# Kernel optimization log

Hardware: AMD Instinct MI355X
Metric: run time of the kernel (lower is better)

The kernel has to match this reference:

```python
import jax, jax.numpy as jnp
import numpy as np

B, T, C, H, D = 2, 2048, 1024, 16, 64

def setup_inputs() -> dict:
    key = jax.random.key(0)
    ks = jax.random.split(key, 5)
    s = 1.0 / np.sqrt(C)
    return {
        "hidden_states": jax.random.normal(ks[0], (B, T, C), jnp.float32),
        "Wq": jax.random.normal(ks[1], (H, C, D), jnp.float32) * s,
        "Wk": jax.random.normal(ks[2], (H, C, D), jnp.float32) * s,
        "Wv": jax.random.normal(ks[3], (H, C, D), jnp.float32) * s,
        "Wo": jax.random.normal(ks[4], (C, C), jnp.float32) * s,
    }

def reference(hidden_states, Wq, Wk, Wv, Wo):
    x = hidden_states  # (B, T, C)
    q = jnp.einsum("btc,hcd->bhtd", x, Wq)
    k = jnp.einsum("btc,hcd->bhtd", x, Wk)
    v = jnp.einsum("btc,hcd->bhtd", x, Wv)
    scale = 1.0 / jnp.sqrt(jnp.asarray(D, x.dtype))
    scores = jnp.einsum("bhtd,bhsd->bhts", q, k) * scale  # (B,H,T,T)
    Tlen = x.shape[1]
    causal = jnp.tril(jnp.ones((Tlen, Tlen), bool))
    scores = jnp.where(causal, scores, jnp.asarray(-jnp.inf, x.dtype))
    probs = jax.nn.softmax(scores, axis=-1)
    heads = jnp.einsum("bhts,bhsd->bhtd", probs, v)  # (B,H,T,D)
    concat = heads.transpose(0, 2, 1, 3).reshape(x.shape[0], Tlen, H * D)  # (B,T,C)
    return jnp.einsum("btc,oc->bto", concat, Wo)  # output projection (dropout=0)
```

## Files before the change

### kernel.cpp

```cpp
#include <hip/hip_runtime.h>
#include <math.h>

#define B_ 2
#define T_ 2048
#define C_ 1024
#define H_ 16
#define D_ 64

typedef short short8 __attribute__((ext_vector_type(8)));
typedef float f32x4 __attribute__((ext_vector_type(4)));

#define LOG2E 1.44269504088896f

__device__ __forceinline__ unsigned short f2bf(float f) {
    unsigned int u = __float_as_uint(f);
    u += 0x7FFFu + ((u >> 16) & 1u);
    return (unsigned short)(u >> 16);
}

#define NCAST 2560

__global__ __launch_bounds__(256) void prep_all(
    const float* __restrict__ x,  const float* __restrict__ Wq,
    const float* __restrict__ Wk, const float* __restrict__ Wv,
    const float* __restrict__ Wo,
    unsigned short* __restrict__ xb,   unsigned short* __restrict__ Wall,
    unsigned short* __restrict__ wob,  int nX, int nW)
{
    const int bid = blockIdx.x;
    const int tid = threadIdx.x;
    if (bid < NCAST) {
        int i = (bid * 256 + tid) * 8;
        const float* s;
        unsigned short* d;
        if (i < nX) { s = x + i; d = xb + i; }
        else {
            int j = i - nX;
            if (j >= nW) return;
            s = Wo + j; d = wob + j;
        }
        float4 a = *(const float4*)s;
        float4 b = *(const float4*)(s + 4);
        ushort4 o0, o1;
        o0.x = f2bf(a.x); o0.y = f2bf(a.y); o0.z = f2bf(a.z); o0.w = f2bf(a.w);
        o1.x = f2bf(b.x); o1.y = f2bf(b.y); o1.z = f2bf(b.z); o1.w = f2bf(b.w);
        *(ushort4*)d = o0;
        *(ushort4*)(d + 4) = o1;
        return;
    }
    __shared__ float t[64][65];
    const int tb = bid - NCAST;
    const int c0 = (tb & 15) * 64;
    const int h  = (tb >> 4) & 15;
    const int z  = tb >> 8;
    const float* W = (z == 0) ? Wq : (z == 1) ? Wk : Wv;
    unsigned short* Wt = Wall + (size_t)z * H_ * D_ * C_;
    const int r = tid >> 4, c4 = (tid & 15) * 4;
    #pragma unroll
    for (int p = 0; p < 4; p++) {
        int cl = r + p * 16;
        float4 v = *(const float4*)&W[((size_t)h * C_ + c0 + cl) * D_ + c4];
        t[cl][c4 + 0] = v.x; t[cl][c4 + 1] = v.y;
        t[cl][c4 + 2] = v.z; t[cl][c4 + 3] = v.w;
    }
    __syncthreads();
    #pragma unroll
    for (int p = 0; p < 4; p++) {
        int d = r + p * 16;
        ushort4 o;
        o.x = f2bf(t[c4 + 0][d]); o.y = f2bf(t[c4 + 1][d]);
        o.z = f2bf(t[c4 + 2][d]); o.w = f2bf(t[c4 + 3][d]);
        *(ushort4*)&Wt[((size_t)h * D_ + d) * C_ + c0 + c4] = o;
    }
}

__global__ __launch_bounds__(256) void qkv_big(
    const unsigned short* __restrict__ X,
    const unsigned short* __restrict__ Wall,
    unsigned short* __restrict__ Qo,
    unsigned short* __restrict__ Ko,
    unsigned short* __restrict__ Vt)
{
    __shared__ unsigned short As[128][72];
    __shared__ unsigned short Bs[128][72];

    const int m0 = blockIdx.x * 128;
    const int n0 = blockIdx.y * 128;
    const int z  = n0 >> 10;
    const int tid = threadIdx.x;
    const int w = tid >> 6, lane = tid & 63, quad = lane >> 4, l16 = lane & 15;
    const int wm = w & 1, wn = w >> 1;
    const int lrow = tid >> 3, lcol = (tid & 7) * 8;

    f32x4 acc[4][4] = {};

    short8 ar[4], br[4];
    #pragma unroll
    for (int p = 0; p < 4; p++) {
        int r = lrow + p * 32;
        ar[p] = *(const short8*)&X[(size_t)(m0 + r) * C_ + lcol];
        br[p] = *(const short8*)&Wall[(size_t)(n0 + r) * C_ + lcol];
    }

    for (int k0 = 0; k0 < C_; k0 += 64) {
        __syncthreads();
        #pragma unroll
        for (int p = 0; p < 4; p++) {
            int r = lrow + p * 32;
            *(short8*)&As[r][lcol] = ar[p];
            *(short8*)&Bs[r][lcol] = br[p];
        }
        __syncthreads();
        if (k0 + 64 < C_) {
            #pragma unroll
            for (int p = 0; p < 4; p++) {
                int r = lrow + p * 32;
                ar[p] = *(const short8*)&X[(size_t)(m0 + r) * C_ + k0 + 64 + lcol];
                br[p] = *(const short8*)&Wall[(size_t)(n0 + r) * C_ + k0 + 64 + lcol];
            }
        }
        #pragma unroll
        for (int ks = 0; ks < 2; ks++) {
            short8 af[4], bf[4];
            #pragma unroll
            for (int i = 0; i < 4; i++)
                af[i] = *(const short8*)&As[wm * 64 + i * 16 + l16][ks * 32 + quad * 8];
            #pragma unroll
            for (int j = 0; j < 4; j++)
                bf[j] = *(const short8*)&Bs[wn * 64 + j * 16 + l16][ks * 32 + quad * 8];
            #pragma unroll
            for (int i = 0; i < 4; i++)
                #pragma unroll
                for (int j = 0; j < 4; j++)
                    acc[i][j] = __builtin_amdgcn_mfma_f32_16x16x32_bf16(af[i], bf[j], acc[i][j], 0, 0, 0);
        }
    }

    if (z == 2) {
        #pragma unroll
        for (int j = 0; j < 4; j++) {
            const int n = n0 + wn * 64 + j * 16 + l16;
            const int h = (n >> 6) & 15, d = n & 63;
            #pragma unroll
            for (int i = 0; i < 4; i++) {
                const int m = m0 + wm * 64 + i * 16 + quad * 4;
                const int b = m >> 11, t = m & (T_ - 1);
                ushort4 pk;
                pk.x = f2bf(acc[i][j][0]);
                pk.y = f2bf(acc[i][j][1]);
                pk.z = f2bf(acc[i][j][2]);
                pk.w = f2bf(acc[i][j][3]);
                *(ushort4*)&Vt[(((size_t)b * H_ + h) * D_ + d) * T_ + t] = pk;
            }
        }
    } else {
        const float scale = (z == 0) ? 0.125f * LOG2E : 1.0f;
        unsigned short* O = (z == 0) ? Qo : Ko;
        #pragma unroll
        for (int j = 0; j < 4; j++) {
            const int n = n0 + wn * 64 + j * 16 + l16;
            const int h = (n >> 6) & 15, d = n & 63;
            #pragma unroll
            for (int i = 0; i < 4; i++)
                #pragma unroll
                for (int r = 0; r < 4; r++) {
                    const int m = m0 + wm * 64 + i * 16 + quad * 4 + r;
                    const int b = m >> 11, t = m & (T_ - 1);
                    O[(((size_t)b * H_ + h) * T_ + t) * D_ + d] = f2bf(acc[i][j][r] * scale);
                }
        }
    }
}

__global__ __launch_bounds__(512, 4) void flash_mfma(
    const unsigned short* __restrict__ Q,
    const unsigned short* __restrict__ K,
    const unsigned short* __restrict__ Vt,
    unsigned short* __restrict__ CC)
{
    __shared__ unsigned short kst[2][64][72];
    __shared__ unsigned short vts[2][64][72];
    __shared__ unsigned short ps [2][64][72];

    const int pairid = blockIdx.x, h = blockIdx.y, b = blockIdx.z;
    const int tid = threadIdx.x;
    const int g  = tid >> 8;
    const int t2 = tid & 255;
    const int w = t2 >> 6, lane = t2 & 63, quad = lane >> 4, l16 = lane & 15;
    const int lrow = t2 >> 3, lcol = (t2 & 7) * 8;
    const size_t hb  = ((size_t)b * H_ + h) * T_;
    const size_t hbD = ((size_t)b * H_ + h) * D_;

    float* fob = (float*)&kst[0][0][0];
    float* flb = (float*)&ps[0][0][0];

    for (int phase = 0; phase < 2; phase++) {
        const int qb = phase ? 31 - pairid : pairid;
        const int q0 = qb * 64;
        const int nkb = qb + 1;
        const int maxit = (nkb + 1) >> 1;

        short8 qf[2];
        #pragma unroll
        for (int ks = 0; ks < 2; ks++)
            qf[ks] = *(const short8*)&Q[(hb + q0 + w * 16 + l16) * D_ + ks * 32 + quad * 8];

        float l_lane = 0.0f;
        f32x4 o[4] = {};

        short8 kreg[2], vreg[2];
        {
            const int k0 = g * 64;
            #pragma unroll
            for (int p = 0; p < 2; p++) {
                int r = lrow + p * 32;
                kreg[p] = *(const short8*)&K[(hb + k0 + r) * D_ + lcol];
                vreg[p] = *(const short8*)&Vt[(hbD + r) * T_ + k0 + lcol];
            }
        }

        for (int it = 0; it < maxit; it++) {
            const int kb = 2 * it + g;
            const bool act = (kb < nkb);
            __syncthreads();
            if (act) {
                #pragma unroll
                for (int p = 0; p < 2; p++) {
                    int r = lrow + p * 32;
                    *(short8*)&kst[g][r][lcol] = kreg[p];
                    *(short8*)&vts[g][r][lcol] = vreg[p];
                }
            }
            __syncthreads();
            if (kb + 2 < nkb) {
                const int k0n = (kb + 2) * 64;
                #pragma unroll
                for (int p = 0; p < 2; p++) {
                    int r = lrow + p * 32;
                    kreg[p] = *(const short8*)&K[(hb + k0n + r) * D_ + lcol];
                    vreg[p] = *(const short8*)&Vt[(hbD + r) * T_ + k0n + lcol];
                }
            }
            if (act) {
                f32x4 s[4] = {};
                #pragma unroll
                for (int ks = 0; ks < 2; ks++)
                    #pragma unroll
                    for (int ct = 0; ct < 4; ct++) {
                        short8 kf = *(const short8*)&kst[g][ct * 16 + l16][ks * 32 + quad * 8];
                        s[ct] = __builtin_amdgcn_mfma_f32_16x16x32_bf16(kf, qf[ks], s[ct], 0, 0, 0);
                    }

                if (kb == qb) {
                    #pragma unroll
                    for (int ct = 0; ct < 4; ct++)
                        #pragma unroll
                        for (int r = 0; r < 4; r++)
                            if (ct * 16 + quad * 4 + r > w * 16 + l16) s[ct][r] = -INFINITY;
                }

                #pragma unroll
                for (int ct = 0; ct < 4; ct++) {
                    float e0 = exp2f(s[ct][0]);
                    float e1 = exp2f(s[ct][1]);
                    float e2 = exp2f(s[ct][2]);
                    float e3 = exp2f(s[ct][3]);
                    l_lane += (e0 + e1) + (e2 + e3);
                    uint2 pk;
                    pk.x = __builtin_amdgcn_perm(
                        __float_as_uint(e1) + 0x8000u, __float_as_uint(e0) + 0x8000u, 0x07060302u);
                    pk.y = __builtin_amdgcn_perm(
                        __float_as_uint(e3) + 0x8000u, __float_as_uint(e2) + 0x8000u, 0x07060302u);
                    *(uint2*)&ps[g][w * 16 + l16][ct * 16 + quad * 4] = pk;
                }

                #pragma unroll
                for (int ks = 0; ks < 2; ks++) {
                    short8 pa = *(const short8*)&ps[g][w * 16 + l16][ks * 32 + quad * 8];
                    #pragma unroll
                    for (int ct = 0; ct < 4; ct++) {
                        short8 vf = *(const short8*)&vts[g][ct * 16 + l16][ks * 32 + quad * 8];
                        o[ct] = __builtin_amdgcn_mfma_f32_16x16x32_bf16(pa, vf, o[ct], 0, 0, 0);
                    }
                }
            }
        }

        l_lane += __shfl_xor(l_lane, 16);
        l_lane += __shfl_xor(l_lane, 32);

        __syncthreads();
        if (g == 1) {
            if (lane < 16) flb[w * 16 + lane] = l_lane;
            #pragma unroll
            for (int ct = 0; ct < 4; ct++)
                #pragma unroll
                for (int r = 0; r < 4; r++)
                    fob[(w * 16 + quad * 4 + r) * 68 + ct * 16 + l16] = o[ct][r];
        }
        __syncthreads();
        if (g == 0) {
            float lt = l_lane + flb[w * 16 + l16];
            if (lane < 16) flb[w * 16 + lane] = lt;
            #pragma unroll
            for (int r = 0; r < 4; r++) {
                const int q = w * 16 + quad * 4 + r;
                const float invl = 1.0f / flb[q];
                const int t = q0 + q;
                #pragma unroll
                for (int ct = 0; ct < 4; ct++) {
                    float ov = o[ct][r] + fob[q * 68 + ct * 16 + l16];
                    CC[((size_t)b * T_ + t) * C_ + h * D_ + ct * 16 + l16] = f2bf(ov * invl);
                }
            }
        }
        __syncthreads();
    }
}

__global__ __launch_bounds__(256) void out_big(
    const unsigned short* __restrict__ X,
    const unsigned short* __restrict__ Wob,
    float* __restrict__ out)
{
    __shared__ unsigned short As[128][72];
    __shared__ unsigned short Bs[128][72];

    const int m0 = blockIdx.x * 128;
    const int n0 = blockIdx.y * 128;
    const int tid = threadIdx.x;
    const int w = tid >> 6, lane = tid & 63, quad = lane >> 4, l16 = lane & 15;
    const int wm = w & 1, wn = w >> 1;
    const int lrow = tid >> 3, lcol = (tid & 7) * 8;

    f32x4 acc[4][4] = {};

    short8 ar[4], br[4];
    #pragma unroll
    for (int p = 0; p < 4; p++) {
        int r = lrow + p * 32;
        ar[p] = *(const short8*)&X[(size_t)(m0 + r) * C_ + lcol];
        br[p] = *(const short8*)&Wob[(size_t)(n0 + r) * C_ + lcol];
    }

    for (int k0 = 0; k0 < C_; k0 += 64) {
        __syncthreads();
        #pragma unroll
        for (int p = 0; p < 4; p++) {
            int r = lrow + p * 32;
            *(short8*)&As[r][lcol] = ar[p];
            *(short8*)&Bs[r][lcol] = br[p];
        }
        __syncthreads();
        if (k0 + 64 < C_) {
            #pragma unroll
            for (int p = 0; p < 4; p++) {
                int r = lrow + p * 32;
                ar[p] = *(const short8*)&X[(size_t)(m0 + r) * C_ + k0 + 64 + lcol];
                br[p] = *(const short8*)&Wob[(size_t)(n0 + r) * C_ + k0 + 64 + lcol];
            }
        }
        #pragma unroll
        for (int ks = 0; ks < 2; ks++) {
            short8 af[4], bf[4];
            #pragma unroll
            for (int i = 0; i < 4; i++)
                af[i] = *(const short8*)&As[wm * 64 + i * 16 + l16][ks * 32 + quad * 8];
            #pragma unroll
            for (int j = 0; j < 4; j++)
                bf[j] = *(const short8*)&Bs[wn * 64 + j * 16 + l16][ks * 32 + quad * 8];
            #pragma unroll
            for (int i = 0; i < 4; i++)
                #pragma unroll
                for (int j = 0; j < 4; j++)
                    acc[i][j] = __builtin_amdgcn_mfma_f32_16x16x32_bf16(af[i], bf[j], acc[i][j], 0, 0, 0);
        }
    }

    #pragma unroll
    for (int i = 0; i < 4; i++)
        #pragma unroll
        for (int j = 0; j < 4; j++)
            #pragma unroll
            for (int r = 0; r < 4; r++)
                out[(size_t)(m0 + wm * 64 + i * 16 + quad * 4 + r) * C_ + n0 + wn * 64 + j * 16 + l16] = acc[i][j][r];
}

extern "C" void kernel_launch(void* const* d_in, const int* in_sizes, int n_in,
                              void* d_out, int out_size, void* d_ws, size_t ws_size,
                              hipStream_t stream) {
    const float* x  = (const float*)d_in[0];
    const float* Wq = (const float*)d_in[1];
    const float* Wk = (const float*)d_in[2];
    const float* Wv = (const float*)d_in[3];
    const float* Wo = (const float*)d_in[4];
    float* out = (float*)d_out;

    const size_t nX = (size_t)B_ * T_ * C_;
    const size_t nW = (size_t)H_ * C_ * D_;
    const size_t nQ = (size_t)B_ * H_ * T_ * D_;
    unsigned short* xb   = (unsigned short*)d_ws;
    unsigned short* Wall = xb + nX;
    unsigned short* Wob  = Wall + 3 * nW;
    unsigned short* Qb   = Wob + nW;
    unsigned short* Kb   = Qb + nQ;
    unsigned short* Vtb  = Kb + nQ;
    unsigned short* CCb  = Vtb + nQ;

    prep_all<<<dim3(NCAST + 768), 256, 0, stream>>>(
        x, Wq, Wk, Wv, Wo, xb, Wall, Wob, (int)nX, (int)nW);
    qkv_big<<<dim3(32, 24), 256, 0, stream>>>(xb, Wall, Qb, Kb, Vtb);
    flash_mfma<<<dim3(16, H_, B_), 512, 0, stream>>>(Qb, Kb, Vtb, CCb);
    out_big<<<dim3(32, 8), 256, 0, stream>>>(CCb, Wob, out);
}
```

Before: 178.2 us.

## Split flash attention into one 256-thread block per query tile with XCD swizzle

The flash kernel no longer runs 512-thread blocks that pair query tiles qb and 31-qb and split the KV blocks between two thread groups. It now launches 1024 single-tile blocks of 256 threads, which removes the cross-group merge of partial outputs and row sums through shared memory and halves LDS use per block. The block index is remapped so each XCD handles a contiguous set of heads, for better L2 reuse of K and V, and s_setprio is raised around the MFMA sections. The trade-off is that the causal work is no longer paired for balance, so blocks vary widely in length and scheduling order now decides the tail.

```diff
diff --git a/kernel.cpp b/kernel.cpp
--- a/kernel.cpp
+++ b/kernel.cpp
@@ -172,149 +172,124 @@
     }
 }
 
-__global__ __launch_bounds__(512, 4) void flash_mfma(
+__global__ __launch_bounds__(256, 4) void flash_mfma(
     const unsigned short* __restrict__ Q,
     const unsigned short* __restrict__ K,
     const unsigned short* __restrict__ Vt,
     unsigned short* __restrict__ CC)
 {
-    __shared__ unsigned short kst[2][64][72];
-    __shared__ unsigned short vts[2][64][72];
-    __shared__ unsigned short ps [2][64][72];
-
-    const int pairid = blockIdx.x, h = blockIdx.y, b = blockIdx.z;
+    __shared__ unsigned short kst[64][72];
+    __shared__ unsigned short vts[64][72];
+    __shared__ unsigned short ps [64][72];
+    __shared__ float flb[64];
+
+    const int dd = blockIdx.x;
+    const int W  = (dd & 7) * 128 + (dd >> 3);
+    const int qb = W & 31;
+    const int head = W >> 5;
+    const int h = head & 15, b = head >> 4;
+
     const int tid = threadIdx.x;
-    const int g  = tid >> 8;
-    const int t2 = tid & 255;
-    const int w = t2 >> 6, lane = t2 & 63, quad = lane >> 4, l16 = lane & 15;
-    const int lrow = t2 >> 3, lcol = (t2 & 7) * 8;
+    const int w = tid >> 6, lane = tid & 63, quad = lane >> 4, l16 = lane & 15;
+    const int lrow = tid >> 3, lcol = (tid & 7) * 8;
     const size_t hb  = ((size_t)b * H_ + h) * T_;
     const size_t hbD = ((size_t)b * H_ + h) * D_;
-
-    float* fob = (float*)&kst[0][0][0];
-    float* flb = (float*)&ps[0][0][0];
-
-    for (int phase = 0; phase < 2; phase++) {
-        const int qb = phase ? 31 - pairid : pairid;
-        const int q0 = qb * 64;
-        const int nkb = qb + 1;
-        const int maxit = (nkb + 1) >> 1;
-
-        short8 qf[2];
-        #pragma unroll
-        for (int ks = 0; ks < 2; ks++)
-            qf[ks] = *(const short8*)&Q[(hb + q0 + w * 16 + l16) * D_ + ks * 32 + quad * 8];
-
-        float l_lane = 0.0f;
-        f32x4 o[4] = {};
-
-        short8 kreg[2], vreg[2];
-        {
-            const int k0 = g * 64;
+    const int q0 = qb * 64;
+    const int nkb = qb + 1;
+
+    short8 qf[2];
+    #pragma unroll
+    for (int ks = 0; ks < 2; ks++)
+        qf[ks] = *(const short8*)&Q[(hb + q0 + w * 16 + l16) * D_ + ks * 32 + quad * 8];
+
+    float l_lane = 0.0f;
+    f32x4 o[4] = {};
+
+    short8 kreg[2], vreg[2];
+    #pragma unroll
+    for (int p = 0; p < 2; p++) {
+        int r = lrow + p * 32;
+        kreg[p] = *(const short8*)&K[(hb + r) * D_ + lcol];
+        vreg[p] = *(const short8*)&Vt[(hbD + r) * T_ + lcol];
+    }
+
+    for (int kb = 0; kb < nkb; kb++) {
+        __syncthreads();
+        #pragma unroll
+        for (int p = 0; p < 2; p++) {
+            int r = lrow + p * 32;
+            *(short8*)&kst[r][lcol] = kreg[p];
+            *(short8*)&vts[r][lcol] = vreg[p];
+        }
+        __syncthreads();
+        if (kb + 1 < nkb) {
+            const int k0n = (kb + 1) * 64;
             #pragma unroll
             for (int p = 0; p < 2; p++) {
                 int r = lrow + p * 32;
-                kreg[p] = *(const short8*)&K[(hb + k0 + r) * D_ + lcol];
-                vreg[p] = *(const short8*)&Vt[(hbD + r) * T_ + k0 + lcol];
-            }
-        }
-
-        for (int it = 0; it < maxit; it++) {
-            const int kb = 2 * it + g;
-            const bool act = (kb < nkb);
-            __syncthreads();
-            if (act) {
-                #pragma unroll
-                for (int p = 0; p < 2; p++) {
-                    int r = lrow + p * 32;
-                    *(short8*)&kst[g][r][lcol] = kreg[p];
-                    *(short8*)&vts[g][r][lcol] = vreg[p];
-                }
-            }
-            __syncthreads();
-            if (kb + 2 < nkb) {
-                const int k0n = (kb + 2) * 64;
-                #pragma unroll
-                for (int p = 0; p < 2; p++) {
-                    int r = lrow + p * 32;
-                    kreg[p] = *(const short8*)&K[(hb + k0n + r) * D_ + lcol];
-                    vreg[p] = *(const short8*)&Vt[(hbD + r) * T_ + k0n + lcol];
-                }
-            }
-            if (act) {
-                f32x4 s[4] = {};
-                #pragma unroll
-                for (int ks = 0; ks < 2; ks++)
-                    #pragma unroll
-                    for (int ct = 0; ct < 4; ct++) {
-                        short8 kf = *(const short8*)&kst[g][ct * 16 + l16][ks * 32 + quad * 8];
-                        s[ct] = __builtin_amdgcn_mfma_f32_16x16x32_bf16(kf, qf[ks], s[ct], 0, 0, 0);
-                    }
-
-                if (kb == qb) {
-                    #pragma unroll
-                    for (int ct = 0; ct < 4; ct++)
-                        #pragma unroll
-                        for (int r = 0; r < 4; r++)
-                            if (ct * 16 + quad * 4 + r > w * 16 + l16) s[ct][r] = -INFINITY;
-                }
-
-                #pragma unroll
-                for (int ct = 0; ct < 4; ct++) {
-                    float e0 = exp2f(s[ct][0]);
-                    float e1 = exp2f(s[ct][1]);
-                    float e2 = exp2f(s[ct][2]);
-                    float e3 = exp2f(s[ct][3]);
-                    l_lane += (e0 + e1) + (e2 + e3);
-                    uint2 pk;
-                    pk.x = __builtin_amdgcn_perm(
-                        __float_as_uint(e1) + 0x8000u, __float_as_uint(e0) + 0x8000u, 0x07060302u);
-                    pk.y = __builtin_amdgcn_perm(
-                        __float_as_uint(e3) + 0x8000u, __float_as_uint(e2) + 0x8000u, 0x07060302u);
-                    *(uint2*)&ps[g][w * 16 + l16][ct * 16 + quad * 4] = pk;
-                }
-
-                #pragma unroll
-                for (int ks = 0; ks < 2; ks++) {
-                    short8 pa = *(const short8*)&ps[g][w * 16 + l16][ks * 32 + quad * 8];
-                    #pragma unroll
-                    for (int ct = 0; ct < 4; ct++) {
-                        short8 vf = *(const short8*)&vts[g][ct * 16 + l16][ks * 32 + quad * 8];
-                        o[ct] = __builtin_amdgcn_mfma_f32_16x16x32_bf16(pa, vf, o[ct], 0, 0, 0);
-                    }
-                }
-            }
-        }
-
-        l_lane += __shfl_xor(l_lane, 16);
-        l_lane += __shfl_xor(l_lane, 32);
-
-        __syncthreads();
-        if (g == 1) {
-            if (lane < 16) flb[w * 16 + lane] = l_lane;
+                kreg[p] = *(const short8*)&K[(hb + k0n + r) * D_ + lcol];
+                vreg[p] = *(const short8*)&Vt[(hbD + r) * T_ + k0n + lcol];
+            }
+        }
+
+        f32x4 s[4] = {};
+        __builtin_amdgcn_s_setprio(1);
+        #pragma unroll
+        for (int ks = 0; ks < 2; ks++)
+            #pragma unroll
+            for (int ct = 0; ct < 4; ct++) {
+                short8 kf = *(const short8*)&kst[ct * 16 + l16][ks * 32 + quad * 8];
+                s[ct] = __builtin_amdgcn_mfma_f32_16x16x32_bf16(kf, qf[ks], s[ct], 0, 0, 0);
+            }
+        __builtin_amdgcn_s_setprio(0);
+
+        if (kb == qb) {
             #pragma unroll
             for (int ct = 0; ct < 4; ct++)
                 #pragma unroll
                 for (int r = 0; r < 4; r++)
-                    fob[(w * 16 + quad * 4 + r) * 68 + ct * 16 + l16] = o[ct][r];
-        }
-        __syncthreads();
-        if (g == 0) {
-            float lt = l_lane + flb[w * 16 + l16];
-            if (lane < 16) flb[w * 16 + lane] = lt;
-            #pragma unroll
-            for (int r = 0; r < 4; r++) {
-                const int q = w * 16 + quad * 4 + r;
-                const float invl = 1.0f / flb[q];
-                const int t = q0 + q;
-                #pragma unroll
-                for (int ct = 0; ct < 4; ct++) {
-                    float ov = o[ct][r] + fob[q * 68 + ct * 16 + l16];
-                    CC[((size_t)b * T_ + t) * C_ + h * D_ + ct * 16 + l16] = f2bf(ov * invl);
-                }
-            }
-        }
-        __syncthreads();
+                    if (ct * 16 + quad * 4 + r > w * 16 + l16) s[ct][r] = -INFINITY;
+        }
+
+        #pragma unroll
+        for (int ct = 0; ct < 4; ct++) {
+            float e0 = exp2f(s[ct][0]);
+            float e1 = exp2f(s[ct][1]);
+            float e2 = exp2f(s[ct][2]);
+            float e3 = exp2f(s[ct][3]);
+            l_lane += (e0 + e1) + (e2 + e3);
+            uint2 pk;
+            pk.x = __builtin_amdgcn_perm(
+                __float_as_uint(e1) + 0x8000u, __float_as_uint(e0) + 0x8000u, 0x07060302u);
+            pk.y = __builtin_amdgcn_perm(
+                __float_as_uint(e3) + 0x8000u, __float_as_uint(e2) + 0x8000u, 0x07060302u);
+            *(uint2*)&ps[w * 16 + l16][ct * 16 + quad * 4] = pk;
+        }
+
+        __builtin_amdgcn_s_setprio(1);
+        #pragma unroll
+        for (int ks = 0; ks < 2; ks++) {
+            short8 pa = *(const short8*)&ps[w * 16 + l16][ks * 32 + quad * 8];
+            #pragma unroll
+            for (int ct = 0; ct < 4; ct++) {
+                short8 vf = *(const short8*)&vts[ct * 16 + l16][ks * 32 + quad * 8];
+                o[ct] = __builtin_amdgcn_mfma_f32_16x16x32_bf16(pa, vf, o[ct], 0, 0, 0);
+            }
+        }
+        __builtin_amdgcn_s_setprio(0);
+    }
+
+    l_lane += __shfl_xor(l_lane, 16);
+    l_lane += __shfl_xor(l_lane, 32);
+    if (lane < 16) flb[w * 16 + lane] = l_lane;
+    #pragma unroll
+    for (int r = 0; r < 4; r++) {
+        const int q = w * 16 + quad * 4 + r;
+        const float invl = 1.0f / flb[q];
+        const int t = q0 + q;
+        #pragma unroll
+        for (int ct = 0; ct < 4; ct++)
+            CC[((size_t)b * T_ + t) * C_ + h * D_ + ct * 16 + l16] = f2bf(o[ct][r] * invl);
     }
 }
 
@@ -410,6 +385,6 @@
     prep_all<<<dim3(NCAST + 768), 256, 0, stream>>>(
         x, Wq, Wk, Wv, Wo, xb, Wall, Wob, (int)nX, (int)nW);
     qkv_big<<<dim3(32, 24), 256, 0, stream>>>(xb, Wall, Qb, Kb, Vtb);
-    flash_mfma<<<dim3(16, H_, B_), 512, 0, stream>>>(Qb, Kb, Vtb, CCb);
+    flash_mfma<<<dim3(1024), 256, 0, stream>>>(Qb, Kb, Vtb, CCb);
     out_big<<<dim3(32, 8), 256, 0, stream>>>(CCb, Wob, out);
 }
```

New measurement: 196.4 us. +10.2%, slower.
